# Optimization experiments

Hardware: AMD Instinct MI355X
Metric: run time of the kernel (lower is better)

Reference implementation:

```python
import jax, jax.numpy as jnp
import numpy as np

B, N, C, H = 4, 1024, 1024, 16
D = C // H                      # head_dim = 64
FFH = int(int(C * 4.0) * 2 / 3) # 2730
EPS = 1e-6


def rmsnorm(x, w):
    return w * (x * jax.lax.rsqrt(jnp.mean(x * x, axis=-1, keepdims=True) + EPS))


def setup_inputs() -> dict:
    key = jax.random.key(0)
    ks = jax.random.split(key, 12)
    s = 0.02
    return {
        "x": jax.random.normal(ks[0], (B, N, C), jnp.float32),
        "c": jax.random.normal(ks[1], (B, C), jnp.float32),
        "norm1_w": jnp.ones((C,), jnp.float32),
        "norm2_w": jnp.ones((C,), jnp.float32),
        "qkv_w": jax.random.normal(ks[2], (3 * C, C), jnp.float32) * s,
        "qkv_b": jnp.zeros((3 * C,), jnp.float32),
        "q_norm_w": jnp.ones((D,), jnp.float32),
        "k_norm_w": jnp.ones((D,), jnp.float32),
        "proj_w": jax.random.normal(ks[3], (C, C), jnp.float32) * s,
        "proj_b": jnp.zeros((C,), jnp.float32),
        "w12_w": jax.random.normal(ks[4], (2 * FFH, C), jnp.float32) * s,
        "w12_b": jnp.zeros((2 * FFH,), jnp.float32),
        "w3_w": jax.random.normal(ks[5], (C, FFH), jnp.float32) * s,
        "w3_b": jnp.zeros((C,), jnp.float32),
        "ada_w": jax.random.normal(ks[6], (6 * C, C), jnp.float32) * s,
        "ada_b": jnp.zeros((6 * C,), jnp.float32),
    }


def modulate(x, shift, scale):
    return x * (1.0 + scale[:, None, :]) + shift[:, None, :]


def attention(x, qkv_w, qkv_b, q_norm_w, k_norm_w, proj_w, proj_b):
    qkv = x @ qkv_w.T + qkv_b                       # (B,N,3C)
    qkv = qkv.reshape(B, N, 3, H, D)
    q, k, v = qkv[:, :, 0], qkv[:, :, 1], qkv[:, :, 2]   # (B,N,H,D)
    q = jnp.transpose(q, (0, 2, 1, 3))              # (B,H,N,D)
    k = jnp.transpose(k, (0, 2, 1, 3))
    v = jnp.transpose(v, (0, 2, 1, 3))
    q = rmsnorm(q, q_norm_w)
    k = rmsnorm(k, k_norm_w)
    attn = jnp.einsum("bhnd,bhmd->bhnm", q, k) / jnp.sqrt(jnp.float32(D))
    attn = jax.nn.softmax(attn, axis=-1)
    out = jnp.einsum("bhnm,bhmd->bhnd", attn, v)
    out = jnp.transpose(out, (0, 2, 1, 3)).reshape(B, N, C)
    return out @ proj_w.T + proj_b


def swiglu(x, w12_w, w12_b, w3_w, w3_b):
    x12 = x @ w12_w.T + w12_b                       # (B,N,2*FFH)
    x1, x2 = x12[..., :FFH], x12[..., FFH:]
    h = jax.nn.silu(x1) * x2
    return h @ w3_w.T + w3_b


def reference(x, c, norm1_w, norm2_w, qkv_w, qkv_b, q_norm_w, k_norm_w,
              proj_w, proj_b, w12_w, w12_b, w3_w, w3_b, ada_w, ada_b):
    ada = jax.nn.silu(c) @ ada_w.T + ada_b          # (B,6C)
    s1, g1, b1, s2, g2, b2 = jnp.split(ada, 6, axis=-1)
    a = attention(modulate(rmsnorm(x, norm1_w), s1, g1),
                  qkv_w, qkv_b, q_norm_w, k_norm_w, proj_w, proj_b)
    x = x + b1[:, None, :] * a
    m = swiglu(modulate(rmsnorm(x, norm2_w), s2, g2), w12_w, w12_b, w3_w, w3_b)
    x = x + b2[:, None, :] * m
    return x
```

## Files before the change

kernel.cpp:

```cpp
#include <hip/hip_runtime.h>

typedef short s16x8 __attribute__((ext_vector_type(8)));
typedef short s16x4 __attribute__((ext_vector_type(4)));
typedef float f32x4 __attribute__((ext_vector_type(4)));

#define B_   4
#define N_   1024
#define C_   1024
#define H_   16
#define D_   64
#define FFH_ 2730
#define FFP_ 2752
#define FFG_ 5632

__device__ __forceinline__ short f2bf(float f) {
  unsigned u = __float_as_uint(f);
  u += 0x7fff + ((u >> 16) & 1);
  return (short)(unsigned short)(u >> 16);
}
__device__ __forceinline__ float silu(float x) { return x / (1.f + __expf(-x)); }

__device__ __forceinline__ void gload16(const void* g, void* l) {
  __builtin_amdgcn_global_load_lds(
      (const __attribute__((address_space(1))) unsigned*)g,
      (__attribute__((address_space(3))) unsigned*)l, 16, 0, 0);
}

__global__ void cvt_bf(const float* __restrict__ s, short* __restrict__ d, const int n4) {
  for (int i = blockIdx.x * 256 + threadIdx.x; i < n4; i += gridDim.x * 256) {
    const float4 v = ((const float4*)s)[i];
    s16x4 o;
    o[0] = f2bf(v.x); o[1] = f2bf(v.y); o[2] = f2bf(v.z); o[3] = f2bf(v.w);
    *(s16x4*)(d + (size_t)i * 4) = o;
  }
}

__global__ void cvt_w3(const float* __restrict__ s, short* __restrict__ d) {
  const int col = blockIdx.x * 256 + threadIdx.x;
  const int row = blockIdx.y;
  if (col < FFP_)
    d[(size_t)row * FFP_ + col] = (col < FFH_) ? f2bf(s[(size_t)row * FFH_ + col]) : (short)0;
}

__global__ void cvt_w12g(const float* __restrict__ s, short* __restrict__ d) {
  const int R = blockIdx.y;
  const int cb = threadIdx.x * 4;
  const int g = R >> 5, half = (R >> 4) & 1, wi = R & 15;
  const int j = g * 16 + wi;
  s16x4 o;
  if (j < FFH_) {
    const float4 v = *(const float4*)(s + (size_t)(j + half * FFH_) * 1024 + cb);
    o[0] = f2bf(v.x); o[1] = f2bf(v.y); o[2] = f2bf(v.z); o[3] = f2bf(v.w);
  } else {
    o[0] = 0; o[1] = 0; o[2] = 0; o[3] = 0;
  }
  *(s16x4*)(d + (size_t)R * 1024 + cb) = o;
}

__global__ void ada_gemm(const float* __restrict__ c, const float* __restrict__ aw,
                         const float* __restrict__ ab, float* __restrict__ ada) {
  const int j = blockIdx.x;
  const int l = threadIdx.x;
  float acc[4] = {0.f, 0.f, 0.f, 0.f};
  const float4* wr = (const float4*)(aw + (size_t)j * 1024);
  #pragma unroll
  for (int p = 0; p < 4; ++p) {
    const float4 wv = wr[p * 64 + l];
    #pragma unroll
    for (int b = 0; b < 4; ++b) {
      const float4 cv = ((const float4*)(c + b * 1024))[p * 64 + l];
      acc[b] += silu(cv.x) * wv.x + silu(cv.y) * wv.y + silu(cv.z) * wv.z + silu(cv.w) * wv.w;
    }
  }
  #pragma unroll
  for (int b = 0; b < 4; ++b) {
    float a = acc[b];
    #pragma unroll
    for (int m = 1; m < 64; m <<= 1) a += __shfl_xor(a, m);
    if (l == 0) ada[b * 6144 + j] = a + ab[j];
  }
}

__global__ void rmsmod(const float* __restrict__ x, const float* __restrict__ wn,
                       const float* __restrict__ ada, const int sOff, const int gOff,
                       short* __restrict__ out) {
  const int row = blockIdx.x;
  const int b = row >> 10;
  const int t = threadIdx.x;
  const float4 v = ((const float4*)(x + (size_t)row * 1024))[t];
  float ss = v.x * v.x + v.y * v.y + v.z * v.z + v.w * v.w;
  #pragma unroll
  for (int m = 1; m < 64; m <<= 1) ss += __shfl_xor(ss, m);
  __shared__ float red[4];
  if ((t & 63) == 0) red[t >> 6] = ss;
  __syncthreads();
  const float rs = rsqrtf((red[0] + red[1] + red[2] + red[3]) * (1.f / 1024.f) + 1e-6f);
  const int j = t * 4;
  const float* sp = ada + b * 6144 + sOff + j;
  const float* gp = ada + b * 6144 + gOff + j;
  s16x4 o;
  o[0] = f2bf(v.x * rs * wn[j + 0] * (1.f + gp[0]) + sp[0]);
  o[1] = f2bf(v.y * rs * wn[j + 1] * (1.f + gp[1]) + sp[1]);
  o[2] = f2bf(v.z * rs * wn[j + 2] * (1.f + gp[2]) + sp[2]);
  o[3] = f2bf(v.w * rs * wn[j + 3] * (1.f + gp[3]) + sp[3]);
  *(s16x4*)(out + (size_t)row * 1024 + j) = o;
}

template <int EPI>
__launch_bounds__(512, 1)
__global__ void gemm8ph(const short* __restrict__ A, const short* __restrict__ Bt,
                        const int K,
                        const float* __restrict__ bias,
                        short* __restrict__ outB,
                        short* __restrict__ qbO, short* __restrict__ kbO,
                        short* __restrict__ vrO,
                        const float* __restrict__ qnw, const float* __restrict__ knw) {
  __shared__ short Ar[4][256 * 32];
  __shared__ short Br[4][256 * 32];
  const int t = threadIdx.x;
  const int l = t & 63;
  const int w = t >> 6;
  const int wm = w >> 2;
  const int wn = w & 3;

  const int nwg = gridDim.x * gridDim.y;
  int lin = blockIdx.y * gridDim.x + blockIdx.x;
  lin = (lin & 7) * (nwg >> 3) + (lin >> 3);
  const int m0 = (lin / gridDim.x) * 256;
  const int n0 = (lin % gridDim.x) * 256;
  const int S = K >> 5;

  f32x4 acc[8][4];
  const f32x4 z4 = {0.f, 0.f, 0.f, 0.f};
  #pragma unroll
  for (int i = 0; i < 8; ++i)
    #pragma unroll
    for (int j = 0; j < 4; ++j) acc[i][j] = z4;

  const short* aSrc = A + (size_t)(m0 + (l & 15)) * K + (l >> 4) * 8;
  const short* bSrc = Bt + (size_t)(n0 + (l & 15)) * K + (l >> 4) * 8;
  const size_t bstep = (size_t)16 * K;

#define STAGE_A(s)                                                             \
  {                                                                            \
    const int _sl = (s) & 3;                                                   \
    gload16(aSrc + (size_t)(2 * w) * bstep + (s) * 32, &Ar[_sl][(2 * w) * 512]); \
    gload16(aSrc + (size_t)(2 * w + 1) * bstep + (s) * 32, &Ar[_sl][(2 * w + 1) * 512]); \
  }
#define STAGE_B(s)                                                             \
  {                                                                            \
    const int _sl = (s) & 3;                                                   \
    gload16(bSrc + (size_t)(2 * w) * bstep + (s) * 32, &Br[_sl][(2 * w) * 512]); \
    gload16(bSrc + (size_t)(2 * w + 1) * bstep + (s) * 32, &Br[_sl][(2 * w + 1) * 512]); \
  }

  STAGE_A(0); STAGE_B(0); STAGE_A(1); STAGE_B(1);

  for (int s = 0; s < S; ++s) {
    const int sl = s & 3;
    if (s + 1 < S) {
      asm volatile("s_waitcnt vmcnt(4)" ::: "memory");
    } else {
      asm volatile("s_waitcnt vmcnt(0)" ::: "memory");
    }
    __builtin_amdgcn_s_barrier();
    __builtin_amdgcn_sched_barrier(0);

    s16x8 bf[4], af[4];
    #pragma unroll
    for (int nf = 0; nf < 4; ++nf)
      bf[nf] = *(const s16x8*)&Br[sl][(wn * 4 + nf) * 512 + l * 8];
    #pragma unroll
    for (int mf = 0; mf < 4; ++mf)
      af[mf] = *(const s16x8*)&Ar[sl][(wm * 8 + mf) * 512 + l * 8];
    if (s + 2 < S) STAGE_A(s + 2);
    __builtin_amdgcn_s_setprio(1);
    #pragma unroll
    for (int mf = 0; mf < 4; ++mf)
      #pragma unroll
      for (int nf = 0; nf < 4; ++nf)
        acc[mf][nf] = __builtin_amdgcn_mfma_f32_16x16x32_bf16(af[mf], bf[nf], acc[mf][nf], 0, 0, 0);
    __builtin_amdgcn_s_setprio(0);
    __builtin_amdgcn_s_barrier();
    __builtin_amdgcn_sched_barrier(0);

    #pragma unroll
    for (int mf = 0; mf < 4; ++mf)
      af[mf] = *(const s16x8*)&Ar[sl][(wm * 8 + 4 + mf) * 512 + l * 8];
    if (s + 2 < S) STAGE_B(s + 2);
    __builtin_amdgcn_s_setprio(1);
    #pragma unroll
    for (int mf = 0; mf < 4; ++mf)
      #pragma unroll
      for (int nf = 0; nf < 4; ++nf)
        acc[4 + mf][nf] = __builtin_amdgcn_mfma_f32_16x16x32_bf16(af[mf], bf[nf], acc[4 + mf][nf], 0, 0, 0);
    __builtin_amdgcn_s_setprio(0);
  }
#undef STAGE_A
#undef STAGE_B

  if (EPI == 2) {
    const int colB = n0 + wn * 64;
    const int sec = colB >> 10;
    const int hh = (colB >> 6) & 15;
    if (sec < 2) {
      short* dst = sec ? kbO : qbO;
      const float* nw = sec ? knw : qnw;
      const float scl = sec ? 1.f : 0.125f;
      #pragma unroll
      for (int mf = 0; mf < 8; ++mf) {
        #pragma unroll
        for (int i = 0; i < 4; ++i) {
          const int row = m0 + wm * 128 + mf * 16 + ((l >> 4) << 2) + i;
          float vv[4];
          float ss = 0.f;
          #pragma unroll
          for (int nf = 0; nf < 4; ++nf) {
            vv[nf] = acc[mf][nf][i] + bias[colB + nf * 16 + (l & 15)];
            ss += vv[nf] * vv[nf];
          }
          ss += __shfl_xor(ss, 1); ss += __shfl_xor(ss, 2);
          ss += __shfl_xor(ss, 4); ss += __shfl_xor(ss, 8);
          const float rs = rsqrtf(ss * (1.f / 64.f) + 1e-6f) * scl;
          const int bb = row >> 10, nn = row & 1023;
          #pragma unroll
          for (int nf = 0; nf < 4; ++nf) {
            const int d = nf * 16 + (l & 15);
            dst[((size_t)(bb * 16 + hh) * 1024 + nn) * 64 + d] = f2bf(vv[nf] * rs * nw[d]);
          }
        }
      }
    } else {
      #pragma unroll
      for (int mf = 0; mf < 8; ++mf)
        #pragma unroll
        for (int nf = 0; nf < 4; ++nf) {
          const int col = colB + nf * 16 + (l & 15);
          const float bsv = bias[col];
          #pragma unroll
          for (int i = 0; i < 4; ++i) {
            const int row = m0 + wm * 128 + mf * 16 + ((l >> 4) << 2) + i;
            vrO[(size_t)row * 1024 + (col - 2048)] = f2bf(acc[mf][nf][i] + bsv);
          }
        }
    }
  }

  if (EPI == 3) {
    #pragma unroll
    for (int mf = 0; mf < 8; ++mf) {
      const int row = m0 + wm * 128 + mf * 16 + ((l >> 4) << 2);
      #pragma unroll
      for (int p = 0; p < 2; ++p) {
        const int rc = (n0 >> 1) + wn * 32 + p * 16 + (l & 15);
        if (rc < FFP_) {
          const bool real = rc < FFH_;
          const float b1 = real ? bias[rc] : 0.f;
          const float b2 = real ? bias[FFH_ + rc] : 0.f;
          #pragma unroll
          for (int i = 0; i < 4; ++i) {
            float o = 0.f;
            if (real) {
              const float x1 = acc[mf][2 * p][i] + b1;
              const float x2 = acc[mf][2 * p + 1][i] + b2;
              o = silu(x1) * x2;
            }
            outB[(size_t)(row + i) * FFP_ + rc] = f2bf(o);
          }
        }
      }
    }
  }
}

__launch_bounds__(256, 2)
__global__ void gemm2ph(const short* __restrict__ A, const short* __restrict__ Bt,
                        const int K,
                        const float* __restrict__ bias,
                        const float* __restrict__ adav,
                        const float* __restrict__ resid,
                        float* __restrict__ outF) {
  __shared__ short As[2][128 * 64];
  __shared__ short Bs[2][128 * 64];
  const int t = threadIdx.x;
  const int l = t & 63;
  const int w = t >> 6;
  const int wr = (w >> 1) * 64, wc = (w & 1) * 64;

  const int nwg = gridDim.x * gridDim.y;
  int lin = blockIdx.y * gridDim.x + blockIdx.x;
  lin = (lin & 7) * (nwg >> 3) + (lin >> 3);
  const int m0 = (lin / gridDim.x) * 128;
  const int n0 = (lin % gridDim.x) * 128;
  const int nT = K >> 6;

  f32x4 acc[4][4];
  const f32x4 z4 = {0.f, 0.f, 0.f, 0.f};
  #pragma unroll
  for (int i = 0; i < 4; ++i)
    #pragma unroll
    for (int j = 0; j < 4; ++j) acc[i][j] = z4;

  const int lr = l >> 3;
  const int lc = (l & 7) ^ lr;
  const short* gAs = A + (size_t)(m0 + w * 32 + lr) * K + lc * 8;
  const short* gBs = Bt + (size_t)(n0 + w * 32 + lr) * K + lc * 8;
  const int wofs = w * 32 * 64;

#define STAGE_(buf, kt)                                                        \
  do {                                                                         \
    const int _ko = (kt) * 64;                                                 \
    _Pragma("unroll") for (int p = 0; p < 4; ++p) {                            \
      gload16(gAs + (size_t)p * 8 * K + _ko, &As[buf][wofs + p * 8 * 64]);     \
      gload16(gBs + (size_t)p * 8 * K + _ko, &Bs[buf][wofs + p * 8 * 64]);     \
    }                                                                          \
  } while (0)

  STAGE_(0, 0);
  __syncthreads();

  for (int kt = 0; kt < nT; ++kt) {
    const int cur = kt & 1;
    if (kt + 1 < nT) STAGE_(cur ^ 1, kt + 1);
    #pragma unroll
    for (int kk = 0; kk < 2; ++kk) {
      const int c16 = kk * 4 + (l >> 4);
      s16x8 af[4], bfr[4];
      #pragma unroll
      for (int mf = 0; mf < 4; ++mf) {
        const int r = wr + mf * 16 + (l & 15);
        af[mf] = *(const s16x8*)&As[cur][r * 64 + ((c16 ^ (r & 7)) << 3)];
      }
      #pragma unroll
      for (int nf = 0; nf < 4; ++nf) {
        const int r = wc + nf * 16 + (l & 15);
        bfr[nf] = *(const s16x8*)&Bs[cur][r * 64 + ((c16 ^ (r & 7)) << 3)];
      }
      __builtin_amdgcn_s_setprio(1);
      #pragma unroll
      for (int mf = 0; mf < 4; ++mf)
        #pragma unroll
        for (int nf = 0; nf < 4; ++nf)
          acc[mf][nf] = __builtin_amdgcn_mfma_f32_16x16x32_bf16(af[mf], bfr[nf], acc[mf][nf], 0, 0, 0);
      __builtin_amdgcn_s_setprio(0);
    }
    __syncthreads();
  }
#undef STAGE_

  const int bIdx = m0 >> 10;
  #pragma unroll
  for (int mf = 0; mf < 4; ++mf) {
    const int row = m0 + wr + mf * 16 + ((l >> 4) << 2);
    #pragma unroll
    for (int nf = 0; nf < 4; ++nf) {
      const int col = n0 + wc + nf * 16 + (l & 15);
      const float bsv = bias[col];
      const float av = adav[bIdx * 6144 + col];
      #pragma unroll
      for (int i = 0; i < 4; ++i) {
        const float v = acc[mf][nf][i] + bsv;
        outF[(size_t)(row + i) * 1024 + col] =
            resid[(size_t)(row + i) * 1024 + col] + av * v;
      }
    }
  }
}

__global__ void v_trans(const short* __restrict__ vr, short* __restrict__ vt) {
  __shared__ short ld[64][72];
  const int t = threadIdx.x;
  const int bh = blockIdx.y, b = bh >> 4, h = bh & 15;
  const int n0 = blockIdx.x * 64;
  const int nl = t >> 2, cb = (t & 3) * 16;
  const short* src = vr + (size_t)(b * 1024 + n0 + nl) * 1024 + h * 64 + cb;
  *(s16x8*)&ld[nl][cb] = *(const s16x8*)src;
  *(s16x8*)&ld[nl][cb + 8] = *(const s16x8*)(src + 8);
  __syncthreads();
  const int d = t >> 2, np = (t & 3) * 16;
  short* dst = vt + (size_t)(bh * 64 + d) * 1024 + n0 + np;
  s16x8 o0, o1;
  #pragma unroll
  for (int p = 0; p < 8; ++p) { o0[p] = ld[np + p][d]; o1[p] = ld[np + 8 + p][d]; }
  *(s16x8*)dst = o0;
  *(s16x8*)(dst + 8) = o1;
}

__launch_bounds__(256, 2)
__global__ void attn(const short* __restrict__ qb, const short* __restrict__ kb,
                     const short* __restrict__ vt, short* __restrict__ ob) {
  __shared__ short Ks[64 * 64];
  __shared__ short Vs[64 * 64];
  __shared__ short Pl[4][32 * 64];
  const int t = threadIdx.x, l = t & 63, w = t >> 6;
  const int bh = blockIdx.y, b = bh >> 4, h = bh & 15;
  const int q0 = blockIdx.x * 128 + w * 32;
  const short* qp = qb + (size_t)bh * (N_ * D_);
  const short* kp = kb + (size_t)bh * (N_ * D_);
  const short* vp = vt + (size_t)bh * (D_ * N_);

  s16x8 qf[2][2];
  #pragma unroll
  for (int mf = 0; mf < 2; ++mf)
    #pragma unroll
    for (int kk = 0; kk < 2; ++kk)
      qf[mf][kk] = *(const s16x8*)&qp[(q0 + mf * 16 + (l & 15)) * 64 + kk * 32 + ((l >> 4) * 8)];

  f32x4 aco[2][4];
  float rm[2][4], rl[2][4];
  const f32x4 z4 = {0.f, 0.f, 0.f, 0.f};
  #pragma unroll
  for (int mf = 0; mf < 2; ++mf) {
    #pragma unroll
    for (int nd = 0; nd < 4; ++nd) aco[mf][nd] = z4;
    #pragma unroll
    for (int i = 0; i < 4; ++i) { rm[mf][i] = -1e30f; rl[mf][i] = 0.f; }
  }

  const int sr = t >> 2, sc = (t & 3) * 2;
  s16x8 rk[2], rv[2];
  #pragma unroll
  for (int p = 0; p < 2; ++p) {
    rk[p] = *(const s16x8*)&kp[sr * 64 + (sc + p) * 8];
    rv[p] = *(const s16x8*)&vp[sr * 1024 + (sc + p) * 8];
  }

  for (int kt = 0; kt < 16; ++kt) {
    if (kt) __syncthreads();
    #pragma unroll
    for (int p = 0; p < 2; ++p) {
      const int cs = ((sc + p) ^ (sr & 7)) << 3;
      *(s16x8*)&Ks[sr * 64 + cs] = rk[p];
      *(s16x8*)&Vs[sr * 64 + cs] = rv[p];
    }
    __syncthreads();
    if (kt < 15) {
      const int kv0 = (kt + 1) * 64;
      #pragma unroll
      for (int p = 0; p < 2; ++p) {
        rk[p] = *(const s16x8*)&kp[(kv0 + sr) * 64 + (sc + p) * 8];
        rv[p] = *(const s16x8*)&vp[sr * 1024 + kv0 + (sc + p) * 8];
      }
    }

    f32x4 s[2][4];
    #pragma unroll
    for (int mf = 0; mf < 2; ++mf)
      #pragma unroll
      for (int nf = 0; nf < 4; ++nf) s[mf][nf] = z4;

    #pragma unroll
    for (int kk = 0; kk < 2; ++kk) {
      const int c16 = kk * 4 + (l >> 4);
      s16x8 kf[4];
      #pragma unroll
      for (int nf = 0; nf < 4; ++nf) {
        const int r = nf * 16 + (l & 15);
        kf[nf] = *(const s16x8*)&Ks[r * 64 + ((c16 ^ (r & 7)) << 3)];
      }
      __builtin_amdgcn_s_setprio(1);
      #pragma unroll
      for (int mf = 0; mf < 2; ++mf)
        #pragma unroll
        for (int nf = 0; nf < 4; ++nf)
          s[mf][nf] = __builtin_amdgcn_mfma_f32_16x16x32_bf16(qf[mf][kk], kf[nf], s[mf][nf], 0, 0, 0);
      __builtin_amdgcn_s_setprio(0);
    }

    #pragma unroll
    for (int mf = 0; mf < 2; ++mf) {
      #pragma unroll
      for (int i = 0; i < 4; ++i) {
        float pm = fmaxf(fmaxf(s[mf][0][i], s[mf][1][i]), fmaxf(s[mf][2][i], s[mf][3][i]));
        pm = fmaxf(pm, __shfl_xor(pm, 1));
        pm = fmaxf(pm, __shfl_xor(pm, 2));
        pm = fmaxf(pm, __shfl_xor(pm, 4));
        pm = fmaxf(pm, __shfl_xor(pm, 8));
        const float nm = fmaxf(rm[mf][i], pm);
        const float corr = __expf(rm[mf][i] - nm);
        rm[mf][i] = nm;
        float rs = 0.f;
        #pragma unroll
        for (int nf = 0; nf < 4; ++nf) {
          const float p = __expf(s[mf][nf][i] - nm);
          s[mf][nf][i] = p;
          rs += p;
        }
        rs += __shfl_xor(rs, 1);
        rs += __shfl_xor(rs, 2);
        rs += __shfl_xor(rs, 4);
        rs += __shfl_xor(rs, 8);
        rl[mf][i] = rl[mf][i] * corr + rs;
        #pragma unroll
        for (int nd = 0; nd < 4; ++nd) aco[mf][nd][i] *= corr;
      }
    }

    short* pw = &Pl[w][0];
    #pragma unroll
    for (int mf = 0; mf < 2; ++mf)
      #pragma unroll
      for (int nf = 0; nf < 4; ++nf)
        #pragma unroll
        for (int i = 0; i < 4; ++i) {
          const int row = mf * 16 + ((l >> 4) << 2) + i;
          const int col = nf * 16 + (l & 15);
          pw[row * 64 + (((col >> 3) ^ (row & 7)) << 3) + (col & 7)] = f2bf(s[mf][nf][i]);
        }

    #pragma unroll
    for (int kk = 0; kk < 2; ++kk) {
      const int c16 = kk * 4 + (l >> 4);
      s16x8 vf[4];
      #pragma unroll
      for (int nd = 0; nd < 4; ++nd) {
        const int r = nd * 16 + (l & 15);
        vf[nd] = *(const s16x8*)&Vs[r * 64 + ((c16 ^ (r & 7)) << 3)];
      }
      __builtin_amdgcn_s_setprio(1);
      #pragma unroll
      for (int mf = 0; mf < 2; ++mf) {
        const int pr = mf * 16 + (l & 15);
        const s16x8 pf = *(const s16x8*)&pw[pr * 64 + ((c16 ^ (pr & 7)) << 3)];
        #pragma unroll
        for (int nd = 0; nd < 4; ++nd)
          aco[mf][nd] = __builtin_amdgcn_mfma_f32_16x16x32_bf16(pf, vf[nd], aco[mf][nd], 0, 0, 0);
      }
      __builtin_amdgcn_s_setprio(0);
    }
  }

  #pragma unroll
  for (int mf = 0; mf < 2; ++mf)
    #pragma unroll
    for (int i = 0; i < 4; ++i) {
      const float inv = 1.f / rl[mf][i];
      const int row = q0 + mf * 16 + ((l >> 4) << 2) + i;
      #pragma unroll
      for (int nd = 0; nd < 4; ++nd) {
        const int col = h * 64 + nd * 16 + (l & 15);
        ob[(size_t)(b * 1024 + row) * 1024 + col] = f2bf(aco[mf][nd][i] * inv);
      }
    }
}

extern "C" void kernel_launch(void* const* d_in, const int* in_sizes, int n_in,
                              void* d_out, int out_size, void* d_ws, size_t ws_size,
                              hipStream_t stream) {
  const float* x     = (const float*)d_in[0];
  const float* c     = (const float*)d_in[1];
  const float* n1w   = (const float*)d_in[2];
  const float* n2w   = (const float*)d_in[3];
  const float* qkvw  = (const float*)d_in[4];
  const float* qkvb  = (const float*)d_in[5];
  const float* qnw   = (const float*)d_in[6];
  const float* knw   = (const float*)d_in[7];
  const float* projw = (const float*)d_in[8];
  const float* projb = (const float*)d_in[9];
  const float* w12w  = (const float*)d_in[10];
  const float* w12b  = (const float*)d_in[11];
  const float* w3w   = (const float*)d_in[12];
  const float* w3b   = (const float*)d_in[13];
  const float* adaw  = (const float*)d_in[14];
  const float* adab  = (const float*)d_in[15];
  float* outp = (float*)d_out;

  char* ws = (char*)d_ws;
  size_t off = 0;
  auto alloc = [&](size_t bytes) { void* p = ws + off; off += (bytes + 255) & ~(size_t)255; return p; };
  short* WQKV = (short*)alloc(3072ull * 1024 * 2);
  short* WPROJ = (short*)alloc(1024ull * 1024 * 2);
  short* W12G = (short*)alloc((size_t)FFG_ * 1024 * 2);
  short* W3B  = (short*)alloc(1024ull * FFP_ * 2);
  float* ADA  = (float*)alloc(4ull * 6144 * 4);
  short* H1   = (short*)alloc(4096ull * 1024 * 2);
  short* QBF  = (short*)alloc(64ull * 1024 * 64 * 2);
  short* KBF  = (short*)alloc(64ull * 1024 * 64 * 2);
  short* VROW = (short*)alloc(4096ull * 1024 * 2);
  short* VTB  = (short*)alloc(64ull * 64 * 1024 * 2);
  short* OBF  = (short*)alloc(4096ull * 1024 * 2);
  float* X1   = (float*)alloc(4096ull * 1024 * 4);
  short* H2   = (short*)alloc(4096ull * 1024 * 2);
  short* HB   = (short*)alloc(4096ull * FFP_ * 2);

  cvt_bf<<<2048, 256, 0, stream>>>(qkvw, WQKV, 3072 * 1024 / 4);
  cvt_bf<<<1024, 256, 0, stream>>>(projw, WPROJ, 1024 * 1024 / 4);
  cvt_w12g<<<dim3(1, FFG_), 256, 0, stream>>>(w12w, W12G);
  cvt_w3<<<dim3(11, 1024), 256, 0, stream>>>(w3w, W3B);
  ada_gemm<<<6144, 64, 0, stream>>>(c, adaw, adab, ADA);
  rmsmod<<<4096, 256, 0, stream>>>(x, n1w, ADA, 0, 1024, H1);
  gemm8ph<2><<<dim3(12, 16), 512, 0, stream>>>(H1, WQKV, 1024, qkvb,
      nullptr, QBF, KBF, VROW, qnw, knw);
  v_trans<<<dim3(16, 64), 256, 0, stream>>>(VROW, VTB);
  attn<<<dim3(8, 64), 256, 0, stream>>>(QBF, KBF, VTB, OBF);
  gemm2ph<<<dim3(8, 32), 256, 0, stream>>>(OBF, WPROJ, 1024, projb, ADA + 2048, x, X1);
  rmsmod<<<4096, 256, 0, stream>>>(X1, n2w, ADA, 3072, 4096, H2);
  gemm8ph<3><<<dim3(22, 16), 512, 0, stream>>>(H2, W12G, 1024, w12b,
      HB, nullptr, nullptr, nullptr, nullptr, nullptr);
  gemm2ph<<<dim3(8, 32), 256, 0, stream>>>(HB, W3B, FFP_, w3b, ADA + 5120, X1, outp);
}
```

Baseline: 308.4 us.

## Restructure GEMM main loop to double-buffered 64-wide K tiles with phased barriers

Replaces the 4-slot, 32-wide K pipeline with two 64-wide K buffers per operand. Each K tile is consumed in four phased MFMA blocks separated by barriers, and the next tile's A and B loads are issued in the first half. This halves loop iterations and interleaves loads with compute differently. In exchange it adds many more barriers and a full vmcnt(0) drain each iteration, which can expose global load latency, since the prefetch distance drops from two stages to one.

```diff
diff --git a/kernel.cpp b/kernel.cpp
--- a/kernel.cpp
+++ b/kernel.cpp
@@ -109,14 +109,13 @@
 template <int EPI>
 __launch_bounds__(512, 1)
 __global__ void gemm8ph(const short* __restrict__ A, const short* __restrict__ Bt,
-                        const int K,
-                        const float* __restrict__ bias,
+                        const int K, const float* __restrict__ bias,
                         short* __restrict__ outB,
                         short* __restrict__ qbO, short* __restrict__ kbO,
                         short* __restrict__ vrO,
                         const float* __restrict__ qnw, const float* __restrict__ knw) {
-  __shared__ short Ar[4][256 * 32];
-  __shared__ short Br[4][256 * 32];
+  __shared__ short Al[2][256 * 64];
+  __shared__ short Bl[2][256 * 64];
   const int t = threadIdx.x;
   const int l = t & 63;
   const int w = t >> 6;
@@ -128,7 +127,7 @@
   lin = (lin & 7) * (nwg >> 3) + (lin >> 3);
   const int m0 = (lin / gridDim.x) * 256;
   const int n0 = (lin % gridDim.x) * 256;
-  const int S = K >> 5;
+  const int nT = K >> 6;
 
   f32x4 acc[8][4];
   const f32x4 z4 = {0.f, 0.f, 0.f, 0.f};
@@ -137,67 +136,65 @@
     #pragma unroll
     for (int j = 0; j < 4; ++j) acc[i][j] = z4;
 
-  const short* aSrc = A + (size_t)(m0 + (l & 15)) * K + (l >> 4) * 8;
-  const short* bSrc = Bt + (size_t)(n0 + (l & 15)) * K + (l >> 4) * 8;
-  const size_t bstep = (size_t)16 * K;
-
-#define STAGE_A(s)                                                             \
-  {                                                                            \
-    const int _sl = (s) & 3;                                                   \
-    gload16(aSrc + (size_t)(2 * w) * bstep + (s) * 32, &Ar[_sl][(2 * w) * 512]); \
-    gload16(aSrc + (size_t)(2 * w + 1) * bstep + (s) * 32, &Ar[_sl][(2 * w + 1) * 512]); \
-  }
-#define STAGE_B(s)                                                             \
-  {                                                                            \
-    const int _sl = (s) & 3;                                                   \
-    gload16(bSrc + (size_t)(2 * w) * bstep + (s) * 32, &Br[_sl][(2 * w) * 512]); \
-    gload16(bSrc + (size_t)(2 * w + 1) * bstep + (s) * 32, &Br[_sl][(2 * w + 1) * 512]); \
-  }
-
-  STAGE_A(0); STAGE_B(0); STAGE_A(1); STAGE_B(1);
-
-  for (int s = 0; s < S; ++s) {
-    const int sl = s & 3;
-    if (s + 1 < S) {
-      asm volatile("s_waitcnt vmcnt(4)" ::: "memory");
-    } else {
-      asm volatile("s_waitcnt vmcnt(0)" ::: "memory");
-    }
-    __builtin_amdgcn_s_barrier();
-    __builtin_amdgcn_sched_barrier(0);
-
-    s16x8 bf[4], af[4];
-    #pragma unroll
-    for (int nf = 0; nf < 4; ++nf)
-      bf[nf] = *(const s16x8*)&Br[sl][(wn * 4 + nf) * 512 + l * 8];
-    #pragma unroll
-    for (int mf = 0; mf < 4; ++mf)
-      af[mf] = *(const s16x8*)&Ar[sl][(wm * 8 + mf) * 512 + l * 8];
-    if (s + 2 < S) STAGE_A(s + 2);
-    __builtin_amdgcn_s_setprio(1);
-    #pragma unroll
-    for (int mf = 0; mf < 4; ++mf)
-      #pragma unroll
-      for (int nf = 0; nf < 4; ++nf)
-        acc[mf][nf] = __builtin_amdgcn_mfma_f32_16x16x32_bf16(af[mf], bf[nf], acc[mf][nf], 0, 0, 0);
-    __builtin_amdgcn_s_setprio(0);
-    __builtin_amdgcn_s_barrier();
-    __builtin_amdgcn_sched_barrier(0);
-
-    #pragma unroll
-    for (int mf = 0; mf < 4; ++mf)
-      af[mf] = *(const s16x8*)&Ar[sl][(wm * 8 + 4 + mf) * 512 + l * 8];
-    if (s + 2 < S) STAGE_B(s + 2);
-    __builtin_amdgcn_s_setprio(1);
-    #pragma unroll
-    for (int mf = 0; mf < 4; ++mf)
-      #pragma unroll
-      for (int nf = 0; nf < 4; ++nf)
-        acc[4 + mf][nf] = __builtin_amdgcn_mfma_f32_16x16x32_bf16(af[mf], bf[nf], acc[4 + mf][nf], 0, 0, 0);
-    __builtin_amdgcn_s_setprio(0);
+  const short* aS = A + (size_t)(m0 + w * 16 + (l & 15)) * K + (l >> 4) * 8;
+  const short* bS = Bt + (size_t)(n0 + w * 16 + (l & 15)) * K + (l >> 4) * 8;
+  const size_t hK = (size_t)128 * K;
+
+#define STAGE_A(buf, kt) { const size_t _ko = (size_t)(kt) * 64;               \
+    gload16(aS + _ko,           &Al[buf][(w * 2 + 0) * 512]);                  \
+    gload16(aS + _ko + 32,      &Al[buf][(w * 2 + 1) * 512]);                  \
+    gload16(aS + hK + _ko,      &Al[buf][((8 + w) * 2 + 0) * 512]);            \
+    gload16(aS + hK + _ko + 32, &Al[buf][((8 + w) * 2 + 1) * 512]); }
+#define STAGE_B(buf, kt) { const size_t _ko = (size_t)(kt) * 64;               \
+    gload16(bS + _ko,           &Bl[buf][(w * 2 + 0) * 512]);                  \
+    gload16(bS + _ko + 32,      &Bl[buf][(w * 2 + 1) * 512]);                  \
+    gload16(bS + hK + _ko,      &Bl[buf][((8 + w) * 2 + 0) * 512]);            \
+    gload16(bS + hK + _ko + 32, &Bl[buf][((8 + w) * 2 + 1) * 512]); }
+#define RD_A(g, kk) { _Pragma("unroll") for (int mf = 0; mf < 4; ++mf)         \
+    af[mf] = *(const s16x8*)&Al[cur][((wm * 8 + (g) * 4 + mf) * 2 + (kk)) * 512 + l * 8]; }
+#define RD_B(kk) { _Pragma("unroll") for (int nf = 0; nf < 4; ++nf)            \
+    bf[nf] = *(const s16x8*)&Bl[cur][((wn * 4 + nf) * 2 + (kk)) * 512 + l * 8]; }
+#define MFMA16(base) { __builtin_amdgcn_s_setprio(1);                          \
+    _Pragma("unroll") for (int mf = 0; mf < 4; ++mf)                           \
+    _Pragma("unroll") for (int nf = 0; nf < 4; ++nf)                           \
+      acc[(base) + mf][nf] = __builtin_amdgcn_mfma_f32_16x16x32_bf16(          \
+          af[mf], bf[nf], acc[(base) + mf][nf], 0, 0, 0);                      \
+    __builtin_amdgcn_s_setprio(0); }
+
+  STAGE_A(0, 0); STAGE_B(0, 0);
+  asm volatile("s_waitcnt vmcnt(0)" ::: "memory");
+  __builtin_amdgcn_s_barrier();
+
+  for (int kt = 0; kt < nT; ++kt) {
+    asm volatile("" ::: "memory");
+    const int cur = kt & 1;
+    const bool pre = (kt + 1 < nT);
+    s16x8 af[4], bf[4];
+    RD_B(0); RD_A(0, 0);
+    if (pre) STAGE_A(cur ^ 1, kt + 1);
+    __builtin_amdgcn_s_barrier();
+    MFMA16(0);
+    __builtin_amdgcn_s_barrier();
+    RD_A(1, 0);
+    if (pre) STAGE_B(cur ^ 1, kt + 1);
+    __builtin_amdgcn_s_barrier();
+    MFMA16(4);
+    __builtin_amdgcn_s_barrier();
+    RD_B(1); RD_A(0, 1);
+    __builtin_amdgcn_s_barrier();
+    MFMA16(0);
+    __builtin_amdgcn_s_barrier();
+    RD_A(1, 1);
+    __builtin_amdgcn_s_barrier();
+    MFMA16(4);
+    asm volatile("s_waitcnt vmcnt(0)" ::: "memory");
+    __builtin_amdgcn_s_barrier();
   }
 #undef STAGE_A
 #undef STAGE_B
+#undef RD_A
+#undef RD_B
+#undef MFMA16
 
   if (EPI == 2) {
     const int colB = n0 + wn * 64;
```

New measurement: 341.8 us. 1.11x slower.
